# Optimization experiments

Hardware: AMD Instinct MI355X
Metric: run time of the kernel (lower is better)

## Reference

```python
import jax, jax.numpy as jnp
import numpy as np

H = 8        # heads
W = 64       # window size
SHIFT = True
DIM = 512
SCALE = (DIM // H) ** -0.5


def setup_inputs() -> dict:
    key = jax.random.key(0)
    k1, k2, k3, k4 = jax.random.split(key, 4)
    x = jax.random.normal(k1, (8, 4096, DIM), dtype=jnp.float32)
    w_qkv = jax.random.normal(k2, (3 * DIM, DIM), dtype=jnp.float32) * 0.02
    w_proj = jax.random.normal(k3, (DIM, DIM), dtype=jnp.float32) * 0.02
    b_proj = jax.random.normal(k4, (DIM,), dtype=jnp.float32) * 0.02
    return {"x": x, "w_qkv": w_qkv, "w_proj": w_proj, "b_proj": b_proj}


def reference(x, w_qkv, w_proj, b_proj):
    B, N, C = x.shape
    if SHIFT:
        x = jnp.roll(x, -W // 2, axis=1)
    pad = (W - N % W) % W  # static Python int
    if pad:
        x = jnp.pad(x, ((0, 0), (0, pad), (0, 0)))
    nw = x.shape[1] // W
    xw = x.reshape(B * nw, W, C)                     # (B', W, C)
    qkv = xw @ w_qkv.T                               # (B', W, 3C)
    qkv = qkv.reshape(B * nw, W, 3, H, C // H)
    q, k, v = qkv[:, :, 0], qkv[:, :, 1], qkv[:, :, 2]  # (B', W, H, dh)
    # NOTE: faithful to source -- heads are NOT moved before matmul, so
    # attention is over the head axis: attn shape (B', W, H, H).
    attn = jnp.einsum('bwhd,bwgd->bwhg', q, k) * SCALE
    attn = jax.nn.softmax(attn, axis=-1)
    out = jnp.einsum('bwhg,bwgd->bwhd', attn, v)     # (B', W, H, dh)
    # transpose(1,2) then raw reshape, exactly as torch does (channel scramble)
    out = out.transpose(0, 2, 1, 3).reshape(B * nw, W, C)
    out = out @ w_proj.T + b_proj
    out = out.reshape(B, nw * W, C)[:, :N]
    if SHIFT:
        out = jnp.roll(out, W // 2, axis=1)
    return out
```

## Files before the change

kernel.cpp:

```cpp
#include <hip/hip_runtime.h>
#include <math.h>

typedef __attribute__((ext_vector_type(8))) short short8;
typedef __attribute__((ext_vector_type(4))) float float4v;

#define KDIM  512
#define NQKV  1536

__device__ __forceinline__ unsigned short f2bf(float f) {
    unsigned int u = __float_as_uint(f);
    u += 0x7FFFu + ((u >> 16) & 1u);
    return (unsigned short)(u >> 16);
}
__device__ __forceinline__ float bf2f(unsigned short u) {
    return __uint_as_float(((unsigned int)u) << 16);
}

__device__ __forceinline__ void gl2lds16(const unsigned short* g, unsigned short* l) {
    __builtin_amdgcn_global_load_lds(
        (const __attribute__((address_space(1))) void*)g,
        (__attribute__((address_space(3))) void*)l, 16, 0, 0);
}

__global__ __launch_bounds__(256) void cast_all_kernel(const float* __restrict__ x,
                                                       const float* __restrict__ wqkv,
                                                       const float* __restrict__ wproj,
                                                       unsigned short* __restrict__ xb,
                                                       unsigned short* __restrict__ wqkvb,
                                                       unsigned short* __restrict__ wprojb) {
    if (blockIdx.x < 16384) {
        int tid = blockIdx.x * 256 + threadIdx.x;
        int t = tid >> 7;
        int c = (tid & 127) << 2;
        int b = t >> 12, n = t & 4095;
        int src = (b << 12) | ((n + 32) & 4095);
        float4 v = *(const float4*)(x + (((size_t)src) << 9) + c);
        ushort4 o;
        o.x = f2bf(v.x); o.y = f2bf(v.y); o.z = f2bf(v.z); o.w = f2bf(v.w);
        *(ushort4*)(xb + (((size_t)t) << 9) + c) = o;
    } else {
        int tid = (blockIdx.x - 16384) * 256 + threadIdx.x;
        int e = tid << 2;
        if (e < NQKV * KDIM) {
            float4 v = *(const float4*)(wqkv + e);
            ushort4 o; o.x = f2bf(v.x); o.y = f2bf(v.y); o.z = f2bf(v.z); o.w = f2bf(v.w);
            *(ushort4*)(wqkvb + e) = o;
        } else {
            int e2 = e - NQKV * KDIM;
            float4 v = *(const float4*)(wproj + e2);
            ushort4 o; o.x = f2bf(v.x); o.y = f2bf(v.y); o.z = f2bf(v.z); o.w = f2bf(v.w);
            *(ushort4*)(wprojb + e2) = o;
        }
    }
}

template<int N>
__global__ __launch_bounds__(256, 2) void gemm_kernel(
        const unsigned short* __restrict__ A,
        const unsigned short* __restrict__ B,
        unsigned short* __restrict__ Cb) {
    __shared__ __align__(16) unsigned short As[128 * 64];
    __shared__ __align__(16) unsigned short Bs[128 * 64];
    constexpr int GX  = N / 128;
    constexpr int PER = (GX * 256) / 8;
    const int wgid = blockIdx.y * GX + blockIdx.x;
    const int swz  = (wgid & 7) * PER + (wgid >> 3);
    const int bm = swz / GX;
    const int bn = swz % GX;

    const int tid = threadIdx.x;
    const int wave = tid >> 6, lane = tid & 63;
    const int quad = lane >> 4, l16 = lane & 15;
    const int wm = (wave >> 1) * 64, wn = (wave & 1) * 64;
    const int srow = lane >> 3;
    const int scol = ((lane & 7) ^ srow) * 8;

    float4v acc[4][4] = {};

    const unsigned short* Abase = A + (size_t)(bm * 128) * KDIM;
    const unsigned short* Bbase = B + (size_t)(bn * 128) * KDIM;

    for (int k0 = 0; k0 < KDIM; k0 += 64) {
        #pragma unroll
        for (int j = 0; j < 4; j++) {
            int chunk = j * 4 + wave;
            int row = chunk * 8 + srow;
            gl2lds16(Abase + (size_t)row * KDIM + k0 + scol, As + chunk * 512);
            gl2lds16(Bbase + (size_t)row * KDIM + k0 + scol, Bs + chunk * 512);
        }
        __syncthreads();
        #pragma unroll
        for (int ki = 0; ki < 2; ki++) {
            short8 af[4], bf[4];
            #pragma unroll
            for (int mi = 0; mi < 4; mi++) {
                int r = wm + mi * 16 + l16;
                int blk = (ki * 4 + quad) ^ (l16 & 7);
                af[mi] = *(const short8*)(As + r * 64 + blk * 8);
            }
            #pragma unroll
            for (int ni = 0; ni < 4; ni++) {
                int r = wn + ni * 16 + l16;
                int blk = (ki * 4 + quad) ^ (l16 & 7);
                bf[ni] = *(const short8*)(Bs + r * 64 + blk * 8);
            }
            #pragma unroll
            for (int mi = 0; mi < 4; mi++)
                #pragma unroll
                for (int ni = 0; ni < 4; ni++)
                    acc[mi][ni] = __builtin_amdgcn_mfma_f32_16x16x32_bf16(
                        af[mi], bf[ni], acc[mi][ni], 0, 0, 0);
        }
        __syncthreads();
    }

    #pragma unroll
    for (int mi = 0; mi < 4; mi++) {
        #pragma unroll
        for (int r = 0; r < 4; r++) {
            int m = bm * 128 + wm + mi * 16 + quad * 4 + r;
            #pragma unroll
            for (int ni = 0; ni < 4; ni++) {
                int n = bn * 128 + wn + ni * 16 + l16;
                Cb[(size_t)m * N + n] = f2bf(acc[mi][ni][r]);
            }
        }
    }
}

__global__ __launch_bounds__(512, 2) void attnproj_kernel(
        const unsigned short* __restrict__ qkvb,
        const unsigned short* __restrict__ wprojb,
        const float* __restrict__ bias,
        float* __restrict__ out) {
    __shared__ __align__(16) unsigned short Asf[64 * 512];
    const int tid = threadIdx.x;
    const int win = blockIdx.x;

    {
        const int w = tid >> 3, h = tid & 7;
        const int t = win * 64 + w;
        const unsigned short* base = qkvb + (size_t)t * NQKV;

        float s[8];
        {
            short8 qs[8];
            #pragma unroll
            for (int dc = 0; dc < 8; dc++)
                qs[dc] = *(const short8*)(base + h * 64 + dc * 8);
            float qv[64];
            #pragma unroll
            for (int dc = 0; dc < 8; dc++)
                #pragma unroll
                for (int j = 0; j < 8; j++)
                    qv[dc * 8 + j] = bf2f((unsigned short)qs[dc][j]);
            #pragma unroll
            for (int g = 0; g < 8; g++) {
                const unsigned short* krow = base + 512 + g * 64;
                float acc = 0.f;
                #pragma unroll
                for (int dc = 0; dc < 8; dc++) {
                    short8 ks = *(const short8*)(krow + dc * 8);
                    #pragma unroll
                    for (int j = 0; j < 8; j++)
                        acc += qv[dc * 8 + j] * bf2f((unsigned short)ks[j]);
                }
                s[g] = acc;
            }
        }

        float mx = s[0];
        #pragma unroll
        for (int g = 1; g < 8; g++) mx = fmaxf(mx, s[g]);
        float p[8], sum = 0.f;
        #pragma unroll
        for (int g = 0; g < 8; g++) { p[g] = __expf((s[g] - mx) * 0.125f); sum += p[g]; }
        float inv = 1.f / sum;
        #pragma unroll
        for (int g = 0; g < 8; g++) p[g] *= inv;

        float o[64];
        #pragma unroll
        for (int j = 0; j < 64; j++) o[j] = 0.f;
        #pragma unroll
        for (int g = 0; g < 8; g++) {
            const unsigned short* vrow = base + 1024 + g * 64;
            #pragma unroll
            for (int dc = 0; dc < 8; dc++) {
                short8 vs = *(const short8*)(vrow + dc * 8);
                #pragma unroll
                for (int j = 0; j < 8; j++)
                    o[dc * 8 + j] += p[g] * bf2f((unsigned short)vs[j]);
            }
        }

        int lw = h * 8 + (w >> 3);
        int keyr = (lw ^ (lw >> 3)) & 7;
        unsigned short* dstrow = Asf + lw * 512;
        #pragma unroll
        for (int dc = 0; dc < 8; dc++) {
            short8 pk;
            #pragma unroll
            for (int j = 0; j < 8; j++) pk[j] = (short)f2bf(o[dc * 8 + j]);
            int cb = (w & 7) * 8 + dc;
            *(short8*)(dstrow + ((cb ^ keyr) * 8)) = pk;
        }
    }
    __syncthreads();

    const int wave = tid >> 6, lane = tid & 63;
    const int quad = lane >> 4, l16 = lane & 15;
    const int wc = wave;

    float4v acc[4][4] = {};
    #pragma unroll
    for (int ks = 0; ks < 16; ks++) {
        short8 af[4], bfr[4];
        #pragma unroll
        for (int mi = 0; mi < 4; mi++) {
            int r = mi * 16 + l16;
            int kb = ks * 4 + quad;
            af[mi] = *(const short8*)(Asf + r * 512 + ((kb ^ ((r ^ (r >> 3)) & 7)) * 8));
        }
        #pragma unroll
        for (int ni = 0; ni < 4; ni++) {
            int r = wc * 64 + ni * 16 + l16;
            bfr[ni] = *(const short8*)(wprojb + (size_t)r * KDIM + ks * 32 + quad * 8);
        }
        #pragma unroll
        for (int mi = 0; mi < 4; mi++)
            #pragma unroll
            for (int ni = 0; ni < 4; ni++)
                acc[mi][ni] = __builtin_amdgcn_mfma_f32_16x16x32_bf16(
                    af[mi], bfr[ni], acc[mi][ni], 0, 0, 0);
    }

    #pragma unroll
    for (int mi = 0; mi < 4; mi++) {
        #pragma unroll
        for (int r4 = 0; r4 < 4; r4++) {
            int m = win * 64 + mi * 16 + quad * 4 + r4;
            int b = m >> 12, pp = m & 4095;
            int nrow = (pp + 32) & 4095;
            float* orow = out + (((size_t)((b << 12) | nrow)) << 9);
            #pragma unroll
            for (int ni = 0; ni < 4; ni++) {
                int n = wc * 64 + ni * 16 + l16;
                orow[n] = acc[mi][ni][r4] + bias[n];
            }
        }
    }
}

extern "C" void kernel_launch(void* const* d_in, const int* in_sizes, int n_in,
                              void* d_out, int out_size, void* d_ws, size_t ws_size,
                              hipStream_t stream) {
    const float* x      = (const float*)d_in[0];
    const float* w_qkv  = (const float*)d_in[1];
    const float* w_proj = (const float*)d_in[2];
    const float* b_proj = (const float*)d_in[3];
    float* out = (float*)d_out;

    char* ws = (char*)d_ws;
    unsigned short* xb     = (unsigned short*)(ws);
    unsigned short* wqkvb  = (unsigned short*)(ws + 33554432);
    unsigned short* wprojb = (unsigned short*)(ws + 35127296);
    unsigned short* qkvb   = (unsigned short*)(ws + 35651584);

    cast_all_kernel<<<17408, 256, 0, stream>>>(x, w_qkv, w_proj, xb, wqkvb, wprojb);
    gemm_kernel<NQKV><<<dim3(12, 256), 256, 0, stream>>>(xb, wqkvb, qkvb);
    attnproj_kernel<<<512, 512, 0, stream>>>(qkvb, wprojb, b_proj, out);
}
```

Measured before the change: 248.1 us.

## Stage K/V rows in LDS and split head dim across thread pairs

The attention phase now loads each chunk of 32 tokens' K and V rows into shared memory with async global-to-LDS copies, instead of every thread re-reading all K/V rows from global memory. Each head's 64-wide dot product is split across two lanes, combined with a shuffle, which halves per-thread register arrays. The window is processed in two chunks with extra barriers. The new shared buffer adds about 66 KB of LDS per block, which may stop two 512-thread blocks from fitting on one CU.

```diff
diff --git a/kernel.cpp b/kernel.cpp
--- a/kernel.cpp
+++ b/kernel.cpp
@@ -128,85 +128,103 @@
     }
 }
 
+#define CHUNK 32
+#define KVS   1032
 __global__ __launch_bounds__(512, 2) void attnproj_kernel(
         const unsigned short* __restrict__ qkvb,
         const unsigned short* __restrict__ wprojb,
         const float* __restrict__ bias,
         float* __restrict__ out) {
     __shared__ __align__(16) unsigned short Asf[64 * 512];
+    __shared__ __align__(16) unsigned short KV[CHUNK * KVS];
     const int tid = threadIdx.x;
     const int win = blockIdx.x;
 
     {
-        const int w = tid >> 3, h = tid & 7;
-        const int t = win * 64 + w;
-        const unsigned short* base = qkvb + (size_t)t * NQKV;
-
-        float s[8];
-        {
-            short8 qs[8];
-            #pragma unroll
-            for (int dc = 0; dc < 8; dc++)
-                qs[dc] = *(const short8*)(base + h * 64 + dc * 8);
-            float qv[64];
-            #pragma unroll
-            for (int dc = 0; dc < 8; dc++)
+        const int dh = tid & 1;
+        const int h  = (tid >> 1) & 7;
+        const int tl = tid >> 4;
+
+        for (int c = 0; c < 2; c++) {
+            const int w = c * CHUNK + tl;
+            const int t = win * 64 + w;
+            const unsigned short* base = qkvb + (size_t)t * NQKV;
+
+            short8 qs[4];
+            #pragma unroll
+            for (int dc = 0; dc < 4; dc++)
+                qs[dc] = *(const short8*)(base + h * 64 + dh * 32 + dc * 8);
+
+            #pragma unroll
+            for (int i = 0; i < 8; i++) {
+                int slot = i * 512 + tid;
+                int row = slot >> 7, c8 = slot & 127;
+                gl2lds16(qkvb + (size_t)(win * 64 + c * CHUNK + row) * NQKV + 512 + c8 * 8,
+                         KV + row * KVS + c8 * 8);
+            }
+            __syncthreads();
+
+            const unsigned short* krow = KV + tl * KVS;
+
+            float qv[32];
+            #pragma unroll
+            for (int dc = 0; dc < 4; dc++)
                 #pragma unroll
                 for (int j = 0; j < 8; j++)
                     qv[dc * 8 + j] = bf2f((unsigned short)qs[dc][j]);
+
+            float s[8];
             #pragma unroll
             for (int g = 0; g < 8; g++) {
-                const unsigned short* krow = base + 512 + g * 64;
                 float acc = 0.f;
                 #pragma unroll
-                for (int dc = 0; dc < 8; dc++) {
-                    short8 ks = *(const short8*)(krow + dc * 8);
+                for (int dc = 0; dc < 4; dc++) {
+                    short8 ks = *(const short8*)(krow + g * 64 + dh * 32 + dc * 8);
                     #pragma unroll
                     for (int j = 0; j < 8; j++)
                         acc += qv[dc * 8 + j] * bf2f((unsigned short)ks[j]);
                 }
-                s[g] = acc;
-            }
-        }
-
-        float mx = s[0];
-        #pragma unroll
-        for (int g = 1; g < 8; g++) mx = fmaxf(mx, s[g]);
-        float p[8], sum = 0.f;
-        #pragma unroll
-        for (int g = 0; g < 8; g++) { p[g] = __expf((s[g] - mx) * 0.125f); sum += p[g]; }
-        float inv = 1.f / sum;
-        #pragma unroll
-        for (int g = 0; g < 8; g++) p[g] *= inv;
-
-        float o[64];
-        #pragma unroll
-        for (int j = 0; j < 64; j++) o[j] = 0.f;
-        #pragma unroll
-        for (int g = 0; g < 8; g++) {
-            const unsigned short* vrow = base + 1024 + g * 64;
-            #pragma unroll
-            for (int dc = 0; dc < 8; dc++) {
-                short8 vs = *(const short8*)(vrow + dc * 8);
-                #pragma unroll
-                for (int j = 0; j < 8; j++)
-                    o[dc * 8 + j] += p[g] * bf2f((unsigned short)vs[j]);
-            }
-        }
-
-        int lw = h * 8 + (w >> 3);
-        int keyr = (lw ^ (lw >> 3)) & 7;
-        unsigned short* dstrow = Asf + lw * 512;
-        #pragma unroll
-        for (int dc = 0; dc < 8; dc++) {
-            short8 pk;
-            #pragma unroll
-            for (int j = 0; j < 8; j++) pk[j] = (short)f2bf(o[dc * 8 + j]);
-            int cb = (w & 7) * 8 + dc;
-            *(short8*)(dstrow + ((cb ^ keyr) * 8)) = pk;
-        }
-    }
-    __syncthreads();
+                s[g] = acc + __shfl_xor(acc, 1);
+            }
+
+            float mx = s[0];
+            #pragma unroll
+            for (int g = 1; g < 8; g++) mx = fmaxf(mx, s[g]);
+            float p[8], sum = 0.f;
+            #pragma unroll
+            for (int g = 0; g < 8; g++) { p[g] = __expf((s[g] - mx) * 0.125f); sum += p[g]; }
+            float inv = 1.f / sum;
+            #pragma unroll
+            for (int g = 0; g < 8; g++) p[g] *= inv;
+
+            float o[32];
+            #pragma unroll
+            for (int j = 0; j < 32; j++) o[j] = 0.f;
+            #pragma unroll
+            for (int g = 0; g < 8; g++) {
+                #pragma unroll
+                for (int dc = 0; dc < 4; dc++) {
+                    short8 vs = *(const short8*)(krow + 512 + g * 64 + dh * 32 + dc * 8);
+                    #pragma unroll
+                    for (int j = 0; j < 8; j++)
+                        o[dc * 8 + j] += p[g] * bf2f((unsigned short)vs[j]);
+                }
+            }
+
+            int lw = h * 8 + (w >> 3);
+            int keyr = (lw ^ (lw >> 3)) & 7;
+            unsigned short* dstrow = Asf + lw * 512;
+            #pragma unroll
+            for (int dc = 0; dc < 4; dc++) {
+                short8 pk;
+                #pragma unroll
+                for (int j = 0; j < 8; j++) pk[j] = (short)f2bf(o[dc * 8 + j]);
+                int cb = (w & 7) * 8 + dh * 4 + dc;
+                *(short8*)(dstrow + ((cb ^ keyr) * 8)) = pk;
+            }
+            __syncthreads();
+        }
+    }
 
     const int wave = tid >> 6, lane = tid & 63;
     const int quad = lane >> 4, l16 = lane & 15;
```

Measured after the change: 253.6 us. +2.2%, slower.

## Split attention-projection into half-windows with LDS-staged K/V and lane-split head dims

Applied to the files above, without the earlier changes.

The fused attention+projection kernel now launches two blocks per window, each owning half of the output rows after the channel scramble (four heads' worth). Each thread handles an 8-element slice of head dim and reduces dot products with cross-lane shuffles, instead of one thread computing a full 64-dim head. K/V rows are staged into LDS via global_load_lds in 16-token chunks. The 64-element register arrays go away, so the launch bound targets 4 blocks per CU and the output tile shrinks to 32 rows. It adds more syncthreads, redundant wproj loads per block, and a block-index swizzle.

```diff
diff --git a/kernel.cpp b/kernel.cpp
--- a/kernel.cpp
+++ b/kernel.cpp
@@ -128,96 +128,106 @@
     }
 }
 
-__global__ __launch_bounds__(512, 2) void attnproj_kernel(
+#define KVS 1032
+__global__ __launch_bounds__(512, 4) void attnproj_kernel(
         const unsigned short* __restrict__ qkvb,
         const unsigned short* __restrict__ wprojb,
         const float* __restrict__ bias,
         float* __restrict__ out) {
-    __shared__ __align__(16) unsigned short Asf[64 * 512];
+    __shared__ __align__(16) unsigned short Asf[32 * 512];
+    __shared__ __align__(16) unsigned short KV[16 * KVS];
     const int tid = threadIdx.x;
-    const int win = blockIdx.x;
+    const int bid = blockIdx.x;
+    const int swzb = (bid & 7) * 128 + (bid >> 3);
+    const int win = swzb >> 1, half = swzb & 1;
 
     {
-        const int w = tid >> 3, h = tid & 7;
-        const int t = win * 64 + w;
-        const unsigned short* base = qkvb + (size_t)t * NQKV;
-
-        float s[8];
-        {
-            short8 qs[8];
-            #pragma unroll
-            for (int dc = 0; dc < 8; dc++)
-                qs[dc] = *(const short8*)(base + h * 64 + dc * 8);
-            float qv[64];
-            #pragma unroll
-            for (int dc = 0; dc < 8; dc++)
+        const int dq = tid & 7;
+        const int h  = (tid >> 3) & 3;
+        const int tl = tid >> 5;
+        const int hg = half * 4 + h;
+
+        short8 qs[4];
+        #pragma unroll
+        for (int c = 0; c < 4; c++)
+            qs[c] = *(const short8*)(qkvb + (size_t)(win * 64 + c * 16 + tl) * NQKV
+                                     + hg * 64 + dq * 8);
+
+        #pragma unroll
+        for (int c = 0; c < 4; c++) {
+            #pragma unroll
+            for (int i = 0; i < 4; i++) {
+                int slot = i * 512 + tid;
+                int row = slot >> 7, c8 = slot & 127;
+                gl2lds16(qkvb + (size_t)(win * 64 + c * 16 + row) * NQKV + 512 + c8 * 8,
+                         KV + row * KVS + c8 * 8);
+            }
+            __syncthreads();
+
+            const unsigned short* krow = KV + tl * KVS;
+            const int w = c * 16 + tl;
+
+            float qv[8];
+            #pragma unroll
+            for (int j = 0; j < 8; j++)
+                qv[j] = bf2f((unsigned short)qs[c][j]);
+
+            float s[8];
+            #pragma unroll
+            for (int g = 0; g < 8; g++) {
+                float acc = 0.f;
+                short8 ks = *(const short8*)(krow + g * 64 + dq * 8);
                 #pragma unroll
                 for (int j = 0; j < 8; j++)
-                    qv[dc * 8 + j] = bf2f((unsigned short)qs[dc][j]);
+                    acc += qv[j] * bf2f((unsigned short)ks[j]);
+                acc += __shfl_xor(acc, 1);
+                acc += __shfl_xor(acc, 2);
+                acc += __shfl_xor(acc, 4);
+                s[g] = acc;
+            }
+
+            float mx = s[0];
+            #pragma unroll
+            for (int g = 1; g < 8; g++) mx = fmaxf(mx, s[g]);
+            float p[8], sum = 0.f;
+            #pragma unroll
+            for (int g = 0; g < 8; g++) { p[g] = __expf((s[g] - mx) * 0.125f); sum += p[g]; }
+            float inv = 1.f / sum;
+            #pragma unroll
+            for (int g = 0; g < 8; g++) p[g] *= inv;
+
+            float o[8];
+            #pragma unroll
+            for (int j = 0; j < 8; j++) o[j] = 0.f;
             #pragma unroll
             for (int g = 0; g < 8; g++) {
-                const unsigned short* krow = base + 512 + g * 64;
-                float acc = 0.f;
-                #pragma unroll
-                for (int dc = 0; dc < 8; dc++) {
-                    short8 ks = *(const short8*)(krow + dc * 8);
-                    #pragma unroll
-                    for (int j = 0; j < 8; j++)
-                        acc += qv[dc * 8 + j] * bf2f((unsigned short)ks[j]);
-                }
-                s[g] = acc;
-            }
-        }
-
-        float mx = s[0];
-        #pragma unroll
-        for (int g = 1; g < 8; g++) mx = fmaxf(mx, s[g]);
-        float p[8], sum = 0.f;
-        #pragma unroll
-        for (int g = 0; g < 8; g++) { p[g] = __expf((s[g] - mx) * 0.125f); sum += p[g]; }
-        float inv = 1.f / sum;
-        #pragma unroll
-        for (int g = 0; g < 8; g++) p[g] *= inv;
-
-        float o[64];
-        #pragma unroll
-        for (int j = 0; j < 64; j++) o[j] = 0.f;
-        #pragma unroll
-        for (int g = 0; g < 8; g++) {
-            const unsigned short* vrow = base + 1024 + g * 64;
-            #pragma unroll
-            for (int dc = 0; dc < 8; dc++) {
-                short8 vs = *(const short8*)(vrow + dc * 8);
+                short8 vs = *(const short8*)(krow + 512 + g * 64 + dq * 8);
                 #pragma unroll
                 for (int j = 0; j < 8; j++)
-                    o[dc * 8 + j] += p[g] * bf2f((unsigned short)vs[j]);
-            }
-        }
-
-        int lw = h * 8 + (w >> 3);
-        int keyr = (lw ^ (lw >> 3)) & 7;
-        unsigned short* dstrow = Asf + lw * 512;
-        #pragma unroll
-        for (int dc = 0; dc < 8; dc++) {
+                    o[j] += p[g] * bf2f((unsigned short)vs[j]);
+            }
+
+            int r = h * 8 + (w >> 3);
+            int keyr = (r ^ (r >> 3)) & 7;
             short8 pk;
             #pragma unroll
-            for (int j = 0; j < 8; j++) pk[j] = (short)f2bf(o[dc * 8 + j]);
-            int cb = (w & 7) * 8 + dc;
-            *(short8*)(dstrow + ((cb ^ keyr) * 8)) = pk;
-        }
-    }
-    __syncthreads();
+            for (int j = 0; j < 8; j++) pk[j] = (short)f2bf(o[j]);
+            int cb = (w & 7) * 8 + dq;
+            *(short8*)(Asf + r * 512 + ((cb ^ keyr) * 8)) = pk;
+            __syncthreads();
+        }
+    }
 
     const int wave = tid >> 6, lane = tid & 63;
     const int quad = lane >> 4, l16 = lane & 15;
     const int wc = wave;
 
-    float4v acc[4][4] = {};
+    float4v acc[2][4] = {};
     #pragma unroll
     for (int ks = 0; ks < 16; ks++) {
-        short8 af[4], bfr[4];
-        #pragma unroll
-        for (int mi = 0; mi < 4; mi++) {
+        short8 af[2], bfr[4];
+        #pragma unroll
+        for (int mi = 0; mi < 2; mi++) {
             int r = mi * 16 + l16;
             int kb = ks * 4 + quad;
             af[mi] = *(const short8*)(Asf + r * 512 + ((kb ^ ((r ^ (r >> 3)) & 7)) * 8));
@@ -228,7 +238,7 @@
             bfr[ni] = *(const short8*)(wprojb + (size_t)r * KDIM + ks * 32 + quad * 8);
         }
         #pragma unroll
-        for (int mi = 0; mi < 4; mi++)
+        for (int mi = 0; mi < 2; mi++)
             #pragma unroll
             for (int ni = 0; ni < 4; ni++)
                 acc[mi][ni] = __builtin_amdgcn_mfma_f32_16x16x32_bf16(
@@ -236,10 +246,10 @@
     }
 
     #pragma unroll
-    for (int mi = 0; mi < 4; mi++) {
+    for (int mi = 0; mi < 2; mi++) {
         #pragma unroll
         for (int r4 = 0; r4 < 4; r4++) {
-            int m = win * 64 + mi * 16 + quad * 4 + r4;
+            int m = win * 64 + half * 32 + mi * 16 + quad * 4 + r4;
             int b = m >> 12, pp = m & 4095;
             int nrow = (pp + 32) & 4095;
             float* orow = out + (((size_t)((b << 12) | nrow)) << 9);
@@ -269,5 +279,5 @@
 
     cast_all_kernel<<<17408, 256, 0, stream>>>(x, w_qkv, w_proj, xb, wqkvb, wprojb);
     gemm_kernel<NQKV><<<dim3(12, 256), 256, 0, stream>>>(xb, wqkvb, qkvb);
-    attnproj_kernel<<<512, 512, 0, stream>>>(qkvb, wprojb, b_proj, out);
-}
+    attnproj_kernel<<<1024, 512, 0, stream>>>(qkvb, wprojb, b_proj, out);
+}
```

New measurement: 256.5 us. +3.4%, slower.
